# Optimization experiments

Measured on AMD Instinct MI355X. Metric: run time of the kernel, lower is better.

## Reference

```python
import jax, jax.numpy as jnp
import numpy as np

H_DIM, W_DIM, D_MODEL = 128, 128, 1024
N_HEADS, HEAD_DIM = 16, 64


def setup_inputs() -> dict:
    key = jax.random.key(0)
    ks = jax.random.split(key, 8)
    s = D_MODEL ** -0.5
    return {
        "hidden_state": jax.random.normal(ks[0], (H_DIM, W_DIM, D_MODEL), jnp.float32),
        "attn_mask": jnp.zeros((1, 1, W_DIM, W_DIM), jnp.float32),
        "cos": jax.random.uniform(ks[1], (H_DIM, W_DIM, 1, HEAD_DIM), jnp.float32),
        "sin": jax.random.uniform(ks[2], (H_DIM, W_DIM, 1, HEAD_DIM), jnp.float32),
        "Wq": jax.random.normal(ks[3], (D_MODEL, N_HEADS * HEAD_DIM), jnp.float32) * s,
        "Wk": jax.random.normal(ks[4], (D_MODEL, N_HEADS * HEAD_DIM), jnp.float32) * s,
        "Wv": jax.random.normal(ks[5], (D_MODEL, N_HEADS * HEAD_DIM), jnp.float32) * s,
        "Wo": jax.random.normal(ks[6], (2 * D_MODEL, D_MODEL), jnp.float32) * s,
    }


def _rotate_half(x):
    x1, x2 = jnp.split(x, 2, axis=-1)
    return jnp.concatenate((-x2, x1), axis=-1)


def reference(hidden_state, attn_mask, cos, sin, Wq, Wk, Wv, Wo):
    h, w, d = hidden_state.shape
    Dh = cos.shape[-1]
    nH = d // Dh
    # projections (no bias) + RoPE on q/k
    q = (hidden_state @ Wq).reshape(h, w, nH, Dh)
    k = (hidden_state @ Wk).reshape(h, w, nH, Dh)
    v = (hidden_state @ Wv).reshape(h, w, nH, Dh)
    q = q * cos + _rotate_half(q) * sin
    k = k * cos + _rotate_half(k) * sin
    # NOTE: original divides by sqrt(hidden_size), not sqrt(head_dim)
    scale = jnp.sqrt(jnp.asarray(d, hidden_state.dtype))
    # ---- width attention: (h, w, nH, Dh) -> (h, nH, w, Dh) ----
    qx, kx, vx = (t.transpose(0, 2, 1, 3) for t in (q, k, v))
    sx = jnp.einsum('ahqd,ahkd->ahqk', qx, kx) / scale + attn_mask  # (h, nH, w, w)
    ow = jnp.einsum('ahqk,ahkd->ahqd', jax.nn.softmax(sx, axis=-1), vx)
    w_weights = ow.transpose(0, 2, 1, 3)  # (h, w, nH, Dh)
    # ---- height attention: (h, w, nH, Dh) -> (w, nH, h, Dh) ----
    qy, ky, vy = (t.transpose(1, 2, 0, 3) for t in (q, k, v))
    my = jnp.transpose(attn_mask, (2, 1, 0, 3))
    sy = jnp.einsum('ahqd,ahkd->ahqk', qy, ky) / scale + my  # (w, nH, h, h)
    oh = jnp.einsum('ahqk,ahkd->ahqd', jax.nn.softmax(sy, axis=-1), vy)
    h_weights = oh.transpose(2, 0, 1, 3)  # (h, w, nH, Dh)
    cat = jnp.concatenate([w_weights.reshape(h, w, d), h_weights.reshape(h, w, d)], axis=-1)
    return cat @ Wo
```

## Files before the change

kernel.cpp:

```cpp
#include <hip/hip_runtime.h>

typedef unsigned short u16;
typedef unsigned int   u32;
typedef __bf16 bf16;
typedef bf16  bf16x8 __attribute__((ext_vector_type(8)));
typedef float f32x4  __attribute__((ext_vector_type(4)));

__device__ __forceinline__ u16 bf16u(float f) {
    u32 x = __builtin_bit_cast(u32, f);
    x += 0x7fffu + ((x >> 16) & 1u);
    return (u16)(x >> 16);
}

__device__ __forceinline__ void gl_lds16(const void* g, void* l) {
    __builtin_amdgcn_global_load_lds(
        (const __attribute__((address_space(1))) u32*)g,
        (__attribute__((address_space(3))) u32*)l, 16, 0, 0);
}

__global__ __launch_bounds__(256) void prep_all(
    const float* __restrict__ hidden, ushort4* __restrict__ Xb,
    const float* __restrict__ Wq, const float* __restrict__ Wk,
    const float* __restrict__ Wv, const float* __restrict__ Wo,
    u16* __restrict__ WqkvT, u16* __restrict__ WoT)
{
    const int z = blockIdx.z;
    if (z == 4) {
        const float4* in = (const float4*)hidden;
        int b = blockIdx.y * 32 + blockIdx.x;
#pragma unroll
        for (int it = 0; it < 8; it++) {
            int i = (b << 11) + (it << 8) + threadIdx.x;
            float4 f = in[i];
            ushort4 o;
            o.x = bf16u(f.x); o.y = bf16u(f.y); o.z = bf16u(f.z); o.w = bf16u(f.w);
            Xb[i] = o;
        }
        return;
    }
    const float* W; u16* WT; int rows, cols;
    if (z < 3) {
        if (blockIdx.y >= 32) return;
        W = (z == 0) ? Wq : (z == 1) ? Wk : Wv;
        WT = WqkvT + (size_t)z * 1024 * 1024;
        rows = 1024; cols = 1024;
    } else {
        W = Wo; WT = WoT; rows = 2048; cols = 1024;
    }
    __shared__ float t[32][33];
    int bx = blockIdx.x * 32, by = blockIdx.y * 32;
    int x = threadIdx.x & 31, y = threadIdx.x >> 5;
#pragma unroll
    for (int i = 0; i < 32; i += 8)
        t[y + i][x] = W[(size_t)(by + y + i) * cols + bx + x];
    __syncthreads();
#pragma unroll
    for (int i = 0; i < 32; i += 8)
        WT[(size_t)(bx + y + i) * rows + by + x] = bf16u(t[x][y + i]);
}

#define BAR   __builtin_amdgcn_s_barrier()
#define SB0   __builtin_amdgcn_sched_barrier(0)
#define VM4   asm volatile("s_waitcnt vmcnt(4)" ::: "memory")
#define VM0   asm volatile("s_waitcnt vmcnt(0)" ::: "memory")

__global__ __launch_bounds__(512, 2) void gemm_fat(
    const u16* __restrict__ A, const u16* __restrict__ BT, void* __restrict__ Cout,
    const float* __restrict__ cosp, const float* __restrict__ sinp,
    int M, int N, int K, int mode)
{
    __shared__ u16 Ld[3][16384];
    const int tid = threadIdx.x;
    const int wid = tid >> 6, lane = tid & 63;
    const int nx = gridDim.x;
    const int nwg = nx * gridDim.y;
    const int orig = blockIdx.y * nx + blockIdx.x;
    const int vid = (orig & 7) * (nwg >> 3) + (orig >> 3);
    const int m0 = (vid / nx) << 8, n0 = (vid % nx) << 8;
    const int wr = wid >> 2, wc = wid & 3;

    const int srow = tid >> 2;
    const int sl = (tid & 3) ^ ((srow >> 1) & 3);
    const u16* aS0 = A + (size_t)(m0 + srow) * K + (sl << 3);
    const u16* aS1 = aS0 + (size_t)128 * K;
    const u16* bS0 = BT + (size_t)(n0 + srow) * K + (sl << 3);
    const u16* bS1 = bS0 + (size_t)128 * K;
    const int wdb = wid << 9;
    const int nt = K >> 5;

#define STAGE(T, B_) do { if ((T) < nt) { size_t _ko = (size_t)(T) << 5; \
        gl_lds16(aS0 + _ko, &Ld[B_][wdb]); \
        gl_lds16(aS1 + _ko, &Ld[B_][4096 + wdb]); \
        gl_lds16(bS0 + _ko, &Ld[B_][8192 + wdb]); \
        gl_lds16(bS1 + _ko, &Ld[B_][12288 + wdb]); } } while (0)

    const int phys = ((lane >> 4) ^ ((lane >> 1) & 3)) << 3;
    const int raw = ((wr << 7) + (lane & 15)) << 5;
    const int rbw = (((wc << 6) + (lane & 15)) << 5) + 8192;

    f32x4 acc[8][4] = {};

    STAGE(0, 0); STAGE(1, 1);
    VM4;
    BAR; SB0;

    int b = 0, bs = 2;
    for (int t = 0; t < nt; ++t) {
        const u16* Lb = &Ld[b][0];
        bf16x8 fa[8], fb[4];
#pragma unroll
        for (int ni = 0; ni < 4; ni++)
            fb[ni] = *(const bf16x8*)&Lb[rbw + (ni << 9) + phys];
#pragma unroll
        for (int mi = 0; mi < 8; mi++)
            fa[mi] = *(const bf16x8*)&Lb[raw + (mi << 9) + phys];
        STAGE(t + 2, bs);
        BAR;
        __builtin_amdgcn_s_setprio(1);
#pragma unroll
        for (int mi = 0; mi < 8; mi++)
#pragma unroll
            for (int ni = 0; ni < 4; ni++)
                acc[mi][ni] = __builtin_amdgcn_mfma_f32_16x16x32_bf16(
                    fa[mi], fb[ni], acc[mi][ni], 0, 0, 0);
        __builtin_amdgcn_s_setprio(0);
        if (t + 2 < nt) { VM4; } else { VM0; }
        BAR; SB0;
        b = (b == 2) ? 0 : b + 1;
        bs = (bs == 2) ? 0 : bs + 1;
    }
#undef STAGE

    const int colbase = n0 + (wc << 6) + (lane & 15);
    if (mode == 2) {
        float* C = (float*)Cout;
#pragma unroll
        for (int mi = 0; mi < 8; mi++)
#pragma unroll
            for (int r = 0; r < 4; r++) {
                int m = m0 + (wr << 7) + (mi << 4) + ((lane >> 4) << 2) + r;
                float* row = C + (size_t)m * N + colbase;
#pragma unroll
                for (int ni = 0; ni < 4; ni++) row[ni << 4] = acc[mi][ni][r];
            }
    } else if (n0 < 2048) {
        u16* C = (u16*)Cout;
#pragma unroll
        for (int mi = 0; mi < 8; mi++)
#pragma unroll
            for (int r = 0; r < 4; r++) {
                int m = m0 + (wr << 7) + (mi << 4) + ((lane >> 4) << 2) + r;
                const float* cb = cosp + ((size_t)m << 6);
                const float* sb = sinp + ((size_t)m << 6);
                u16* row = C + (size_t)m * N + colbase;
#pragma unroll
                for (int ni = 0; ni < 4; ni++) {
                    int d = (ni << 4) + (lane & 15);
                    float c = cb[d], s = sb[d];
                    float v0 = acc[mi][ni][r];
                    float vr = acc[mi][ni ^ 2][r];
                    float o = fmaf(v0, c, (ni < 2 ? -vr : vr) * s);
                    row[ni << 4] = bf16u(o);
                }
            }
    } else {
        u16* C = (u16*)Cout;
#pragma unroll
        for (int mi = 0; mi < 8; mi++)
#pragma unroll
            for (int r = 0; r < 4; r++) {
                int m = m0 + (wr << 7) + (mi << 4) + ((lane >> 4) << 2) + r;
                u16* row = C + (size_t)m * N + colbase;
#pragma unroll
                for (int ni = 0; ni < 4; ni++) row[ni << 4] = bf16u(acc[mi][ni][r]);
            }
    }
}

__global__ __launch_bounds__(256) void axial_attn(
    const u16* __restrict__ qkv, const float* __restrict__ mask,
    u16* __restrict__ cat)
{
    __shared__ u16 Kl[128 * 64];
    __shared__ u16 VT[64 * 128];
    __shared__ u16 Pl[128 * 128];
    const int hmode = blockIdx.x >> 11;
    const int o2 = blockIdx.x & 2047;
    const int b = (o2 & 7) * 256 + (o2 >> 3);
    const int a = b >> 4, hd = b & 15;
    const int tid = threadIdx.x, wid = tid >> 6, lane = tid & 63;
    const int tmul = hmode ? 128 : 1;
    const int tadd = hmode ? a : (a << 7);
    const size_t hoff = (size_t)hd << 6;

#pragma unroll
    for (int c = 0; c < 4; c++) {
        int row = (wid << 5) + (c << 3) + (lane >> 3);
        int sc = (lane & 7) ^ (row & 7);
        gl_lds16(qkv + (size_t)(row * tmul + tadd) * 3072 + 1024 + hoff + (sc << 3),
                 &Kl[((wid << 5) + (c << 3)) << 6]);
    }
#pragma unroll
    for (int i = 0; i < 4; i++) {
        int cid = tid + (i << 8);
        int j = cid >> 3;
        int d0 = (cid & 7) << 3;
        uint4 raw = *(const uint4*)(qkv + (size_t)(j * tmul + tadd) * 3072 + 2048 + hoff + d0);
        const u16* e = (const u16*)&raw;
#pragma unroll
        for (int t = 0; t < 8; t++) {
            int d = d0 + t;
            VT[(d << 7) + (((j >> 3) ^ (d & 15)) << 3) + (j & 7)] = e[t];
        }
    }
    bf16x8 aq[2][2];
#pragma unroll
    for (int qt = 0; qt < 2; qt++)
#pragma unroll
        for (int ks = 0; ks < 2; ks++) {
            int row = (wid << 5) + (qt << 4) + (lane & 15);
            aq[qt][ks] = *(const bf16x8*)(qkv + (size_t)(row * tmul + tadd) * 3072 + hoff
                                          + (ks << 5) + ((lane >> 4) << 3));
        }
    __syncthreads();

    f32x4 S[2][8] = {};
#pragma unroll
    for (int kt = 0; kt < 8; kt++) {
        bf16x8 bk[2];
#pragma unroll
        for (int ks = 0; ks < 2; ks++) {
            int row = (kt << 4) + (lane & 15);
            int ch = ((ks << 2) + (lane >> 4)) ^ (row & 7);
            bk[ks] = *(const bf16x8*)&Kl[(row << 6) + (ch << 3)];
        }
#pragma unroll
        for (int qt = 0; qt < 2; qt++) {
            S[qt][kt] = __builtin_amdgcn_mfma_f32_16x16x32_bf16(aq[qt][0], bk[0], S[qt][kt], 0, 0, 0);
            S[qt][kt] = __builtin_amdgcn_mfma_f32_16x16x32_bf16(aq[qt][1], bk[1], S[qt][kt], 0, 0, 0);
        }
    }

    const float scale = 0.03125f;
#pragma unroll
    for (int qt = 0; qt < 2; qt++) {
#pragma unroll
        for (int r = 0; r < 4; r++) {
            int qrow = (wid << 5) + (qt << 4) + ((lane >> 4) << 2) + r;
            const float* mrow = mask + (hmode ? (a << 7) : (qrow << 7));
            float mx = -1e30f;
#pragma unroll
            for (int kt = 0; kt < 8; kt++) {
                float sv = fmaf(S[qt][kt][r], scale, mrow[(kt << 4) + (lane & 15)]);
                S[qt][kt][r] = sv;
                mx = fmaxf(mx, sv);
            }
            mx = fmaxf(mx, __shfl_xor(mx, 1));
            mx = fmaxf(mx, __shfl_xor(mx, 2));
            mx = fmaxf(mx, __shfl_xor(mx, 4));
            mx = fmaxf(mx, __shfl_xor(mx, 8));
            float sum = 0.f;
#pragma unroll
            for (int kt = 0; kt < 8; kt++) {
                float p = __expf(S[qt][kt][r] - mx);
                S[qt][kt][r] = p;
                sum += p;
            }
            sum += __shfl_xor(sum, 1);
            sum += __shfl_xor(sum, 2);
            sum += __shfl_xor(sum, 4);
            sum += __shfl_xor(sum, 8);
            float rinv = 1.0f / sum;
#pragma unroll
            for (int kt = 0; kt < 8; kt++) {
                int kcol = (kt << 4) + (lane & 15);
                int ch = (kcol >> 3) ^ (qrow & 15);
                Pl[(qrow << 7) + (ch << 3) + (kcol & 7)] = bf16u(S[qt][kt][r] * rinv);
            }
        }
    }
    __syncthreads();

    f32x4 O[4][2] = {};
#pragma unroll
    for (int ks = 0; ks < 4; ks++) {
        bf16x8 av[4], bp[2];
#pragma unroll
        for (int qt = 0; qt < 2; qt++) {
            int qrow = (wid << 5) + (qt << 4) + (lane & 15);
            int ch = ((ks << 2) + (lane >> 4)) ^ (qrow & 15);
            bp[qt] = *(const bf16x8*)&Pl[(qrow << 7) + (ch << 3)];
        }
#pragma unroll
        for (int dt = 0; dt < 4; dt++) {
            int drow = (dt << 4) + (lane & 15);
            int ch = ((ks << 2) + (lane >> 4)) ^ (drow & 15);
            av[dt] = *(const bf16x8*)&VT[(drow << 7) + (ch << 3)];
        }
#pragma unroll
        for (int dt = 0; dt < 4; dt++)
#pragma unroll
            for (int qt = 0; qt < 2; qt++)
                O[dt][qt] = __builtin_amdgcn_mfma_f32_16x16x32_bf16(av[dt], bp[qt], O[dt][qt], 0, 0, 0);
    }

    const int cbase = (hmode ? 1024 : 0) + (hd << 6);
#pragma unroll
    for (int dt = 0; dt < 4; dt++)
#pragma unroll
        for (int qt = 0; qt < 2; qt++) {
            int qrow = (wid << 5) + (qt << 4) + (lane & 15);
            int d0 = (dt << 4) + ((lane >> 4) << 2);
            size_t base = ((size_t)(qrow * tmul + tadd) << 11) + cbase + d0;
            ushort4 pk;
            pk.x = bf16u(O[dt][qt][0]);
            pk.y = bf16u(O[dt][qt][1]);
            pk.z = bf16u(O[dt][qt][2]);
            pk.w = bf16u(O[dt][qt][3]);
            *(ushort4*)(cat + base) = pk;
        }
}

extern "C" void kernel_launch(void* const* d_in, const int* in_sizes, int n_in,
                              void* d_out, int out_size, void* d_ws, size_t ws_size,
                              hipStream_t stream)
{
    (void)in_sizes; (void)n_in; (void)out_size; (void)ws_size;
    const float* hidden = (const float*)d_in[0];
    const float* mask   = (const float*)d_in[1];
    const float* cosp   = (const float*)d_in[2];
    const float* sinp   = (const float*)d_in[3];
    const float* Wq     = (const float*)d_in[4];
    const float* Wk     = (const float*)d_in[5];
    const float* Wv     = (const float*)d_in[6];
    const float* Wo     = (const float*)d_in[7];

    char* ws = (char*)d_ws;
    u16* Xb    = (u16*)(ws);
    u16* WqkvT = (u16*)(ws + 33554432);
    u16* cat   = (u16*)(ws);
    u16* WoT   = (u16*)(ws + 67108864);
    u16* qkvb  = (u16*)(ws + 71303168);

    prep_all<<<dim3(32, 64, 5), 256, 0, stream>>>(hidden, (ushort4*)Xb,
                                                  Wq, Wk, Wv, Wo, WqkvT, WoT);

    gemm_fat<<<dim3(12, 64), 512, 0, stream>>>(Xb, WqkvT, qkvb, cosp, sinp, 16384, 3072, 1024, 1);

    axial_attn<<<4096, 256, 0, stream>>>(qkvb, mask, cat);

    gemm_fat<<<dim3(4, 64), 512, 0, stream>>>(cat, WoT, d_out, nullptr, nullptr, 16384, 1024, 2048, 2);
}
```

Baseline: 318.4 us.

## Retile GEMMs to 128x256 with 4 waves and alias attention LDS buffers

The 256x256, 512-thread GEMM becomes a 128x256 tile run by 256 threads. Each wave now computes 64x128, and a new 2D XCD-aware block swizzle places blocks on the chiplets. The axial attention kernel shares one LDS buffer: P overwrites the K region after a new barrier, and V transpose stores are packed two elements per 32-bit write. The aim is higher occupancy and better L2 locality, plus lower LDS footprint and fewer LDS stores in attention. In exchange, operand reuse per tile drops, the GEMM issues more loads per MFMA, and attention gains an extra sync.

```diff
diff --git a/kernel.cpp b/kernel.cpp
--- a/kernel.cpp
+++ b/kernel.cpp
@@ -61,118 +61,123 @@
 
 #define BAR   __builtin_amdgcn_s_barrier()
 #define SB0   __builtin_amdgcn_sched_barrier(0)
-#define VM4   asm volatile("s_waitcnt vmcnt(4)" ::: "memory")
+#define VM6   asm volatile("s_waitcnt vmcnt(6)" ::: "memory")
 #define VM0   asm volatile("s_waitcnt vmcnt(0)" ::: "memory")
 
-__global__ __launch_bounds__(512, 2) void gemm_fat(
+#define XCD2D2(SHM, SHN) \
+    const int nx = gridDim.x, ny = gridDim.y; \
+    const int orig = blockIdx.y * nx + blockIdx.x; \
+    const int xcd = orig & 7, idx = orig >> 3; \
+    const int nxh = nx >> 1; \
+    const int m0 = ((xcd >> 1) * (ny >> 2) + idx / nxh) << (SHM); \
+    const int n0 = ((xcd & 1) * nxh + idx % nxh) << (SHN);
+
+__global__ __launch_bounds__(256, 2) void gemm_wn(
     const u16* __restrict__ A, const u16* __restrict__ BT, void* __restrict__ Cout,
     const float* __restrict__ cosp, const float* __restrict__ sinp,
     int M, int N, int K, int mode)
 {
-    __shared__ u16 Ld[3][16384];
+    __shared__ u16 Ld[3][12288];
     const int tid = threadIdx.x;
     const int wid = tid >> 6, lane = tid & 63;
-    const int nx = gridDim.x;
-    const int nwg = nx * gridDim.y;
-    const int orig = blockIdx.y * nx + blockIdx.x;
-    const int vid = (orig & 7) * (nwg >> 3) + (orig >> 3);
-    const int m0 = (vid / nx) << 8, n0 = (vid % nx) << 8;
-    const int wr = wid >> 2, wc = wid & 3;
+    XCD2D2(7, 8)
+    const int wr = wid >> 1, wc = wid & 1;
 
     const int srow = tid >> 2;
-    const int sl = (tid & 3) ^ ((srow >> 1) & 3);
-    const u16* aS0 = A + (size_t)(m0 + srow) * K + (sl << 3);
-    const u16* aS1 = aS0 + (size_t)128 * K;
-    const u16* bS0 = BT + (size_t)(n0 + srow) * K + (sl << 3);
-    const u16* bS1 = bS0 + (size_t)128 * K;
+    const int sg = (tid & 3) ^ ((srow >> 1) & 3);
+    const u16* aS = A + (size_t)(m0 + srow) * K + (sg << 3);
+    const u16* bS = BT + (size_t)(n0 + srow) * K + (sg << 3);
+    const size_t h64K = (size_t)64 * K;
     const int wdb = wid << 9;
     const int nt = K >> 5;
 
-#define STAGE(T, B_) do { if ((T) < nt) { size_t _ko = (size_t)(T) << 5; \
-        gl_lds16(aS0 + _ko, &Ld[B_][wdb]); \
-        gl_lds16(aS1 + _ko, &Ld[B_][4096 + wdb]); \
-        gl_lds16(bS0 + _ko, &Ld[B_][8192 + wdb]); \
-        gl_lds16(bS1 + _ko, &Ld[B_][12288 + wdb]); } } while (0)
+#define STAGE(T, B_) do { if ((T) < nt) { const size_t _ko = (size_t)(T) << 5; \
+        gl_lds16(aS + _ko,            &Ld[B_][wdb]); \
+        gl_lds16(aS + _ko + h64K,     &Ld[B_][2048 + wdb]); \
+        gl_lds16(bS + _ko,            &Ld[B_][4096 + wdb]); \
+        gl_lds16(bS + _ko + h64K,     &Ld[B_][6144 + wdb]); \
+        gl_lds16(bS + _ko + 2 * h64K, &Ld[B_][8192 + wdb]); \
+        gl_lds16(bS + _ko + 3 * h64K, &Ld[B_][10240 + wdb]); } } while (0)
 
     const int phys = ((lane >> 4) ^ ((lane >> 1) & 3)) << 3;
-    const int raw = ((wr << 7) + (lane & 15)) << 5;
-    const int rbw = (((wc << 6) + (lane & 15)) << 5) + 8192;
-
-    f32x4 acc[8][4] = {};
+    const int raw = ((wr << 6) + (lane & 15)) << 5;
+    const int rbw = 4096 + (((wc << 7) + (lane & 15)) << 5);
+
+    f32x4 acc[4][8] = {};
 
     STAGE(0, 0); STAGE(1, 1);
-    VM4;
+    VM6;
     BAR; SB0;
 
     int b = 0, bs = 2;
     for (int t = 0; t < nt; ++t) {
         const u16* Lb = &Ld[b][0];
-        bf16x8 fa[8], fb[4];
-#pragma unroll
-        for (int ni = 0; ni < 4; ni++)
+        bf16x8 fa[4], fb[8];
+#pragma unroll
+        for (int ni = 0; ni < 8; ni++)
             fb[ni] = *(const bf16x8*)&Lb[rbw + (ni << 9) + phys];
 #pragma unroll
-        for (int mi = 0; mi < 8; mi++)
+        for (int mi = 0; mi < 4; mi++)
             fa[mi] = *(const bf16x8*)&Lb[raw + (mi << 9) + phys];
         STAGE(t + 2, bs);
         BAR;
         __builtin_amdgcn_s_setprio(1);
 #pragma unroll
-        for (int mi = 0; mi < 8; mi++)
-#pragma unroll
-            for (int ni = 0; ni < 4; ni++)
+        for (int mi = 0; mi < 4; mi++)
+#pragma unroll
+            for (int ni = 0; ni < 8; ni++)
                 acc[mi][ni] = __builtin_amdgcn_mfma_f32_16x16x32_bf16(
                     fa[mi], fb[ni], acc[mi][ni], 0, 0, 0);
         __builtin_amdgcn_s_setprio(0);
-        if (t + 2 < nt) { VM4; } else { VM0; }
+        if (t + 2 < nt) { VM6; } else { VM0; }
         BAR; SB0;
         b = (b == 2) ? 0 : b + 1;
         bs = (bs == 2) ? 0 : bs + 1;
     }
 #undef STAGE
 
-    const int colbase = n0 + (wc << 6) + (lane & 15);
+    const int colbase = n0 + (wc << 7) + (lane & 15);
     if (mode == 2) {
         float* C = (float*)Cout;
 #pragma unroll
-        for (int mi = 0; mi < 8; mi++)
+        for (int mi = 0; mi < 4; mi++)
 #pragma unroll
             for (int r = 0; r < 4; r++) {
-                int m = m0 + (wr << 7) + (mi << 4) + ((lane >> 4) << 2) + r;
+                int m = m0 + (wr << 6) + (mi << 4) + ((lane >> 4) << 2) + r;
                 float* row = C + (size_t)m * N + colbase;
 #pragma unroll
-                for (int ni = 0; ni < 4; ni++) row[ni << 4] = acc[mi][ni][r];
+                for (int ni = 0; ni < 8; ni++) row[ni << 4] = acc[mi][ni][r];
             }
     } else if (n0 < 2048) {
         u16* C = (u16*)Cout;
 #pragma unroll
-        for (int mi = 0; mi < 8; mi++)
+        for (int mi = 0; mi < 4; mi++)
 #pragma unroll
             for (int r = 0; r < 4; r++) {
-                int m = m0 + (wr << 7) + (mi << 4) + ((lane >> 4) << 2) + r;
+                int m = m0 + (wr << 6) + (mi << 4) + ((lane >> 4) << 2) + r;
                 const float* cb = cosp + ((size_t)m << 6);
                 const float* sb = sinp + ((size_t)m << 6);
                 u16* row = C + (size_t)m * N + colbase;
 #pragma unroll
-                for (int ni = 0; ni < 4; ni++) {
-                    int d = (ni << 4) + (lane & 15);
+                for (int ni = 0; ni < 8; ni++) {
+                    int d = ((ni & 3) << 4) + (lane & 15);
                     float c = cb[d], s = sb[d];
                     float v0 = acc[mi][ni][r];
                     float vr = acc[mi][ni ^ 2][r];
-                    float o = fmaf(v0, c, (ni < 2 ? -vr : vr) * s);
+                    float o = fmaf(v0, c, ((ni & 3) < 2 ? -vr : vr) * s);
                     row[ni << 4] = bf16u(o);
                 }
             }
     } else {
         u16* C = (u16*)Cout;
 #pragma unroll
-        for (int mi = 0; mi < 8; mi++)
+        for (int mi = 0; mi < 4; mi++)
 #pragma unroll
             for (int r = 0; r < 4; r++) {
-                int m = m0 + (wr << 7) + (mi << 4) + ((lane >> 4) << 2) + r;
+                int m = m0 + (wr << 6) + (mi << 4) + ((lane >> 4) << 2) + r;
                 u16* row = C + (size_t)m * N + colbase;
 #pragma unroll
-                for (int ni = 0; ni < 4; ni++) row[ni << 4] = bf16u(acc[mi][ni][r]);
+                for (int ni = 0; ni < 8; ni++) row[ni << 4] = bf16u(acc[mi][ni][r]);
             }
     }
 }
@@ -181,9 +186,7 @@
     const u16* __restrict__ qkv, const float* __restrict__ mask,
     u16* __restrict__ cat)
 {
-    __shared__ u16 Kl[128 * 64];
-    __shared__ u16 VT[64 * 128];
-    __shared__ u16 Pl[128 * 128];
+    __shared__ u16 sh[24576];
     const int hmode = blockIdx.x >> 11;
     const int o2 = blockIdx.x & 2047;
     const int b = (o2 & 7) * 256 + (o2 >> 3);
@@ -198,19 +201,23 @@
         int row = (wid << 5) + (c << 3) + (lane >> 3);
         int sc = (lane & 7) ^ (row & 7);
         gl_lds16(qkv + (size_t)(row * tmul + tadd) * 3072 + 1024 + hoff + (sc << 3),
-                 &Kl[((wid << 5) + (c << 3)) << 6]);
-    }
-#pragma unroll
-    for (int i = 0; i < 4; i++) {
-        int cid = tid + (i << 8);
-        int j = cid >> 3;
-        int d0 = (cid & 7) << 3;
-        uint4 raw = *(const uint4*)(qkv + (size_t)(j * tmul + tadd) * 3072 + 2048 + hoff + d0);
-        const u16* e = (const u16*)&raw;
+                 &sh[((wid << 5) + (c << 3)) << 6]);
+    }
+#pragma unroll
+    for (int i = 0; i < 2; i++) {
+        int pid = tid + (i << 8);
+        int j0 = (pid >> 3) << 1, j1 = j0 | 1;
+        int d0 = (pid & 7) << 3;
+        uint4 r0 = *(const uint4*)(qkv + (size_t)(j0 * tmul + tadd) * 3072 + 2048 + hoff + d0);
+        uint4 r1 = *(const uint4*)(qkv + (size_t)(j1 * tmul + tadd) * 3072 + 2048 + hoff + d0);
+        const u16* e0 = (const u16*)&r0;
+        const u16* e1 = (const u16*)&r1;
+        int g = j0 >> 3, lo = j0 & 7;
 #pragma unroll
         for (int t = 0; t < 8; t++) {
             int d = d0 + t;
-            VT[(d << 7) + (((j >> 3) ^ (d & 15)) << 3) + (j & 7)] = e[t];
+            *(u32*)&sh[8192 + (d << 7) + ((g ^ (d & 15)) << 3) + lo] =
+                (u32)e0[t] | ((u32)e1[t] << 16);
         }
     }
     bf16x8 aq[2][2];
@@ -232,7 +239,7 @@
         for (int ks = 0; ks < 2; ks++) {
             int row = (kt << 4) + (lane & 15);
             int ch = ((ks << 2) + (lane >> 4)) ^ (row & 7);
-            bk[ks] = *(const bf16x8*)&Kl[(row << 6) + (ch << 3)];
+            bk[ks] = *(const bf16x8*)&sh[(row << 6) + (ch << 3)];
         }
 #pragma unroll
         for (int qt = 0; qt < 2; qt++) {
@@ -240,6 +247,7 @@
             S[qt][kt] = __builtin_amdgcn_mfma_f32_16x16x32_bf16(aq[qt][1], bk[1], S[qt][kt], 0, 0, 0);
         }
     }
+    __syncthreads();
 
     const float scale = 0.03125f;
 #pragma unroll
@@ -247,6 +255,7 @@
 #pragma unroll
         for (int r = 0; r < 4; r++) {
             int qrow = (wid << 5) + (qt << 4) + ((lane >> 4) << 2) + r;
+            const int plb = (qrow << 7) + ((qrow & 64) ? 8192 : 0);
             const float* mrow = mask + (hmode ? (a << 7) : (qrow << 7));
             float mx = -1e30f;
 #pragma unroll
@@ -275,7 +284,7 @@
             for (int kt = 0; kt < 8; kt++) {
                 int kcol = (kt << 4) + (lane & 15);
                 int ch = (kcol >> 3) ^ (qrow & 15);
-                Pl[(qrow << 7) + (ch << 3) + (kcol & 7)] = bf16u(S[qt][kt][r] * rinv);
+                sh[plb + (ch << 3) + (kcol & 7)] = bf16u(S[qt][kt][r] * rinv);
             }
         }
     }
@@ -289,13 +298,13 @@
         for (int qt = 0; qt < 2; qt++) {
             int qrow = (wid << 5) + (qt << 4) + (lane & 15);
             int ch = ((ks << 2) + (lane >> 4)) ^ (qrow & 15);
-            bp[qt] = *(const bf16x8*)&Pl[(qrow << 7) + (ch << 3)];
+            bp[qt] = *(const bf16x8*)&sh[(qrow << 7) + ((qrow & 64) ? 8192 : 0) + (ch << 3)];
         }
 #pragma unroll
         for (int dt = 0; dt < 4; dt++) {
             int drow = (dt << 4) + (lane & 15);
             int ch = ((ks << 2) + (lane >> 4)) ^ (drow & 15);
-            av[dt] = *(const bf16x8*)&VT[(drow << 7) + (ch << 3)];
+            av[dt] = *(const bf16x8*)&sh[8192 + (drow << 7) + (ch << 3)];
         }
 #pragma unroll
         for (int dt = 0; dt < 4; dt++)
@@ -345,9 +354,9 @@
     prep_all<<<dim3(32, 64, 5), 256, 0, stream>>>(hidden, (ushort4*)Xb,
                                                   Wq, Wk, Wv, Wo, WqkvT, WoT);
 
-    gemm_fat<<<dim3(12, 64), 512, 0, stream>>>(Xb, WqkvT, qkvb, cosp, sinp, 16384, 3072, 1024, 1);
+    gemm_wn<<<dim3(12, 128), 256, 0, stream>>>(Xb, WqkvT, qkvb, cosp, sinp, 16384, 3072, 1024, 1);
 
     axial_attn<<<4096, 256, 0, stream>>>(qkvb, mask, cat);
 
-    gemm_fat<<<dim3(4, 64), 512, 0, stream>>>(cat, WoT, d_out, nullptr, nullptr, 16384, 1024, 2048, 2);
-}
+    gemm_wn<<<dim3(4, 128), 256, 0, stream>>>(cat, WoT, d_out, nullptr, nullptr, 16384, 1024, 2048, 2);
+}
```

Result: faster. 298.7 us, median of 2 (-6.2%).
